# Kernel tuning notes

Hardware: AMD Instinct MI355X
Metric: run time of the kernel (lower is better)

## Reference

```python
import jax, jax.numpy as jnp
import numpy as np

D_MODEL = 1024
NUM_HEADS = 16
HEAD_DIM = D_MODEL // NUM_HEADS
LN_EPS = 1e-3  # keras LayerNormalization default epsilon


def setup_inputs() -> dict:
    key = jax.random.key(0)
    ks = jax.random.split(key, 10)
    B, T = 2, 2048
    s = 1.0 / np.sqrt(D_MODEL)
    return {
        "x": jax.random.normal(ks[0], (B, T, D_MODEL), dtype=jnp.float32),
        "Wq": jax.random.normal(ks[1], (D_MODEL, D_MODEL), dtype=jnp.float32) * s,
        "Wk": jax.random.normal(ks[2], (D_MODEL, D_MODEL), dtype=jnp.float32) * s,
        "Wv": jax.random.normal(ks[3], (D_MODEL, D_MODEL), dtype=jnp.float32) * s,
        "Wg": jax.random.normal(ks[4], (D_MODEL, D_MODEL), dtype=jnp.float32) * s,
        "bg": jnp.zeros((D_MODEL,), dtype=jnp.float32),
        "Wo": jax.random.normal(ks[5], (D_MODEL, D_MODEL), dtype=jnp.float32) * s,
        "bo": jnp.zeros((D_MODEL,), dtype=jnp.float32),
        "ln_gamma": jnp.ones((D_MODEL,), dtype=jnp.float32),
        "ln_beta": jnp.zeros((D_MODEL,), dtype=jnp.float32),
    }


def reference(x, Wq, Wk, Wv, Wg, bg, Wo, bo, ln_gamma, ln_beta):
    B, T, D = x.shape
    H, dh = NUM_HEADS, HEAD_DIM

    def split_heads(z):
        return z.reshape(B, T, H, dh).transpose(0, 2, 1, 3)  # [B,H,T,dh]

    Q = split_heads(x @ Wq)
    K = split_heads(x @ Wk)
    V = split_heads(x @ Wv)
    G = jax.nn.swish(x @ Wg + bg)  # [B,T,D]

    # Per-head causal decay mask D[h,m,n] = gamma_h^(m-n) for m>=n else 0
    idx = jnp.arange(T, dtype=jnp.float32)
    diff = idx[:, None] - idx[None, :]  # [T,T]
    causal = (diff >= 0).astype(jnp.float32)
    gammas = 1.0 - 2.0 ** (-5.0 - jnp.arange(H, dtype=jnp.float32))  # [H]
    Dmask = (gammas[:, None, None] ** jnp.maximum(diff, 0.0)) * causal  # [H,T,T]

    scale = float(dh) ** 0.5
    scores = jnp.einsum('bhtd,bhsd->bhts', Q, K) / scale  # [B,H,T,T]
    ret = jnp.einsum('bhts,bhsd->bhtd', scores * Dmask[None], V)  # [B,H,T,dh]
    ret = ret.transpose(0, 2, 1, 3).reshape(B, T, D)  # concat heads

    # LayerNorm (axis=-1, keras default eps=1e-3)
    mu = jnp.mean(ret, axis=-1, keepdims=True)
    var = jnp.mean(jnp.square(ret - mu), axis=-1, keepdims=True)
    ln = (ret - mu) / jnp.sqrt(var + LN_EPS) * ln_gamma + ln_beta

    return (ln * G) @ Wo + bo
```

## Files before the change

### kernel.cpp

```cpp
#include <hip/hip_runtime.h>

#define D_MODEL 1024
#define NHEADS  16
#define HDIM    64
#define BATCH   2
#define SEQ     2048
#define ROWS    (BATCH*SEQ)
#define CHUNK   128
#define NCHUNK  (SEQ/CHUNK)
#define LN_EPS  1e-3f

typedef unsigned short ushort_t;
typedef __attribute__((ext_vector_type(4))) float          f32x4;
typedef __attribute__((ext_vector_type(8))) short          s16x8;
typedef __attribute__((ext_vector_type(4))) unsigned short u16x4;
typedef __attribute__((ext_vector_type(8))) unsigned short u16x8;

__device__ __forceinline__ ushort_t f2b(float f) {
    union { float f; unsigned int u; } v; v.f = f;
    unsigned int r = v.u + 0x7fffu + ((v.u >> 16) & 1u);
    return (ushort_t)(r >> 16);
}
__device__ __forceinline__ float b2f(ushort_t b) {
    union { unsigned int u; float f; } v; v.u = ((unsigned int)b) << 16;
    return v.f;
}

__device__ __forceinline__ void async_load16(const ushort_t* g, ushort_t* l) {
    __builtin_amdgcn_global_load_lds(
        (const __attribute__((address_space(1))) unsigned int*)(g),
        (__attribute__((address_space(3))) unsigned int*)(l),
        16, 0, 0);
}

__global__ __launch_bounds__(256) void cast_x_kernel(const float* __restrict__ x,
                                                     ushort_t* __restrict__ xb) {
    int idx = (blockIdx.x * 256 + threadIdx.x) * 4;
    f32x4 v = *(const f32x4*)(x + idx);
    u16x4 o;
    o.x = f2b(v.x); o.y = f2b(v.y); o.z = f2b(v.z); o.w = f2b(v.w);
    *(u16x4*)(xb + idx) = o;
}

__global__ __launch_bounds__(256) void wt_transpose_kernel(
        const float* __restrict__ Wq, const float* __restrict__ Wk,
        const float* __restrict__ Wv, const float* __restrict__ Wg,
        const float* __restrict__ Wo,
        ushort_t* __restrict__ WcatT, ushort_t* __restrict__ WoT) {
    __shared__ float tile[32][33];
    int z = blockIdx.z;
    const float* W = (z == 0) ? Wq : (z == 1) ? Wk : (z == 2) ? Wv : (z == 3) ? Wg : Wo;
    ushort_t* dst = (z < 4) ? (WcatT + (size_t)z * 1024 * 1024) : WoT;
    int n0 = blockIdx.x * 32, k0 = blockIdx.y * 32;
    int tx = threadIdx.x, ty = threadIdx.y;
#pragma unroll
    for (int i = 0; i < 4; i++) {
        int k = k0 + ty + i * 8;
        tile[ty + i * 8][tx] = W[(size_t)k * 1024 + n0 + tx];
    }
    __syncthreads();
#pragma unroll
    for (int i = 0; i < 4; i++) {
        int n = n0 + ty + i * 8;
        dst[(size_t)n * 1024 + k0 + tx] = f2b(tile[tx][ty + i * 8]);
    }
}

__global__ __launch_bounds__(256, 2) void gemm_kernel(
        const ushort_t* __restrict__ A, const ushort_t* __restrict__ BT,
        int K, int N, int mode, const float* __restrict__ bias,
        ushort_t* __restrict__ Yout, float* __restrict__ Fout) {
    extern __shared__ char smem[];
    ushort_t* As = (ushort_t*)smem;
    ushort_t* Bs = As + 128 * 64;
    int t = threadIdx.x;
    int row0 = blockIdx.y * 128, col0 = blockIdx.x * 128;
    int w = t >> 6, lane = t & 63;
    int wr = (w >> 1) * 64, wc = (w & 1) * 64;
    int qd = lane >> 4, ln = lane & 15;
    int lx = ln & 7;

    f32x4 acc[4][4];
#pragma unroll
    for (int i = 0; i < 4; i++)
#pragma unroll
        for (int j = 0; j < 4; j++) acc[i][j] = (f32x4)0.0f;

    for (int k0 = 0; k0 < K; k0 += 64) {
#pragma unroll
        for (int p = 0; p < 4; p++) {
            int g = p * 256 + t;
            int r = g >> 3;
            int kb = g & 7;
            int kbs = kb ^ (r & 7);
            async_load16(A + (size_t)(row0 + r) * K + k0 + kbs * 8, As + g * 8);
            async_load16(BT + (size_t)(col0 + r) * K + k0 + kbs * 8, Bs + g * 8);
        }
        __syncthreads();
#pragma unroll
        for (int kk = 0; kk < 64; kk += 32) {
            s16x8 af[4], bf[4];
            int kxa = ((kk >> 3) + qd) ^ lx;
#pragma unroll
            for (int i = 0; i < 4; i++)
                af[i] = *(const s16x8*)(As + (wr + i * 16 + ln) * 64 + kxa * 8);
#pragma unroll
            for (int j = 0; j < 4; j++)
                bf[j] = *(const s16x8*)(Bs + (wc + j * 16 + ln) * 64 + kxa * 8);
#pragma unroll
            for (int i = 0; i < 4; i++)
#pragma unroll
                for (int j = 0; j < 4; j++)
                    acc[i][j] = __builtin_amdgcn_mfma_f32_16x16x32_bf16(
                        af[i], bf[j], acc[i][j], 0, 0, 0);
        }
        __syncthreads();
    }

#pragma unroll
    for (int i = 0; i < 4; i++)
#pragma unroll
        for (int j = 0; j < 4; j++) {
            int n = col0 + wc + j * 16 + ln;
#pragma unroll
            for (int r = 0; r < 4; r++) {
                int m = row0 + wr + i * 16 + qd * 4 + r;
                float v = acc[i][j][r];
                if (mode == 0) {
                    int region = n >> 10;
                    if (region == 0) v *= 0.125f;
                    else if (region == 3) {
                        v += bias[n & 1023];
                        v = v / (1.0f + __expf(-v));
                    }
                    Yout[(size_t)m * N + n] = f2b(v);
                } else {
                    Fout[(size_t)m * N + n] = v + bias[n];
                }
            }
        }
}

#define SJ 136
__global__ __launch_bounds__(256) void chunk_states_kernel(const ushort_t* __restrict__ Y,
                                                           float* __restrict__ Astate) {
    __shared__ ushort_t Ktd[64 * SJ];
    __shared__ ushort_t Vtd[64 * SJ];
    int c = blockIdx.x, h = blockIdx.y, b = blockIdx.z;
    int t = threadIdx.x;
    float gamma = 1.0f - exp2f(-5.0f - (float)h);
    float l2g = log2f(gamma);
    int row0 = b * SEQ + c * CHUNK;
    int colK = D_MODEL + h * HDIM;

    for (int g = t; g < 1024; g += 256) {
        int j = g >> 3, dg = (g & 7) * 8;
        size_t src = (size_t)(row0 + j) * 4096 + colK + dg;
        u16x8 k8 = *(const u16x8*)(Y + src);
        u16x8 v8 = *(const u16x8*)(Y + src + D_MODEL);
        float dec = exp2f((float)(127 - j) * l2g);
#pragma unroll
        for (int q = 0; q < 8; q++) {
            Ktd[(dg + q) * SJ + j] = f2b(b2f(k8[q]) * dec);
            Vtd[(dg + q) * SJ + j] = v8[q];
        }
    }
    __syncthreads();

    int w = t >> 6, lane = t & 63;
    int wr = w * 16;
    int qd = lane >> 4, ln = lane & 15;

    s16x8 af[4];
#pragma unroll
    for (int ks = 0; ks < 4; ks++)
        af[ks] = *(const s16x8*)(Ktd + (wr + ln) * SJ + ks * 32 + qd * 8);

    f32x4 acc[4];
#pragma unroll
    for (int nt = 0; nt < 4; nt++) {
        acc[nt] = (f32x4)0.0f;
#pragma unroll
        for (int ks = 0; ks < 4; ks++) {
            s16x8 bf = *(const s16x8*)(Vtd + (nt * 16 + ln) * SJ + ks * 32 + qd * 8);
            acc[nt] = __builtin_amdgcn_mfma_f32_16x16x32_bf16(af[ks], bf, acc[nt], 0, 0, 0);
        }
    }

    size_t base = ((size_t)((b * NHEADS + h) * NCHUNK + c)) * 4096;
#pragma unroll
    for (int nt = 0; nt < 4; nt++)
#pragma unroll
        for (int r = 0; r < 4; r++)
            Astate[base + (size_t)(wr + qd * 4 + r) * 64 + nt * 16 + ln] = acc[nt][r];
}

__global__ __launch_bounds__(256) void scan_kernel(const float* __restrict__ Astate,
                                                   float* __restrict__ Sprev) {
    int h = blockIdx.x, b = blockIdx.y;
    int bh = b * NHEADS + h;
    float gamma = 1.0f - exp2f(-5.0f - (float)h);
    float gC = exp2f(128.0f * log2f(gamma));
    for (int g = threadIdx.x; g < 1024; g += 256) {
        f32x4 S = (f32x4)0.0f;
        for (int c = 0; c < NCHUNK; c++) {
            size_t off = ((size_t)bh * NCHUNK + c) * 4096 + g * 4;
            *(f32x4*)(Sprev + off) = S;
            f32x4 Ain = *(const f32x4*)(Astate + off);
            S = S * gC + Ain;
        }
    }
}

#define LDW 72
#define VT_LDW 136
#define CO_ELEMS (128*LDW*2 + 64*LDW*2 + 64*VT_LDW)
__global__ __launch_bounds__(256, 2) void chunk_out_kernel(const ushort_t* __restrict__ Y,
                                                           const float* __restrict__ Sprev,
                                                           float* __restrict__ ret) {
    extern __shared__ char smem[];
    ushort_t* Qs   = (ushort_t*)smem;
    ushort_t* Kc   = Qs + 128 * LDW;
    ushort_t* Sphi = Kc + 128 * LDW;
    ushort_t* Splo = Sphi + 64 * LDW;
    ushort_t* Vt   = Splo + 64 * LDW;
    ushort_t* Pl   = Qs;

    int c = blockIdx.x, h = blockIdx.y, b = blockIdx.z;
    int t = threadIdx.x;
    float gamma = 1.0f - exp2f(-5.0f - (float)h);
    float l2g = log2f(gamma);
    int row0 = b * SEQ + c * CHUNK;

    for (int g = t; g < 1024; g += 256) {
        int i = g >> 3, dg = (g & 7) * 8;
        size_t src = (size_t)(row0 + i) * 4096 + h * HDIM + dg;
        *(u16x8*)(Qs + i * LDW + dg) = *(const u16x8*)(Y + src);
        *(u16x8*)(Kc + i * LDW + dg) = *(const u16x8*)(Y + src + D_MODEL);
        u16x8 v = *(const u16x8*)(Y + src + 2 * D_MODEL);
#pragma unroll
        for (int k2 = 0; k2 < 8; k2++) Vt[(dg + k2) * VT_LDW + i] = v[k2];
    }
    {
        size_t sbase = ((size_t)((b * NHEADS + h) * NCHUNK + c)) * 4096;
        for (int g = t; g < 1024; g += 256) {
            int e = g >> 4, dg = (g & 15) * 4;
            f32x4 s4 = *(const f32x4*)(Sprev + sbase + e * 64 + dg);
#pragma unroll
            for (int k2 = 0; k2 < 4; k2++) {
                float s = s4[k2];
                ushort_t hb = f2b(s);
                float lo = s - b2f(hb);
                Sphi[(dg + k2) * LDW + e] = hb;
                Splo[(dg + k2) * LDW + e] = f2b(lo);
            }
        }
    }
    __syncthreads();

    int w = t >> 6, lane = t & 63;
    int wr = w * 32;
    int qd = lane >> 4, ln = lane & 15;

    s16x8 aq[2][2];
#pragma unroll
    for (int mt = 0; mt < 2; mt++)
#pragma unroll
        for (int ks = 0; ks < 2; ks++)
            aq[mt][ks] = *(const s16x8*)(Qs + (wr + mt * 16 + ln) * LDW + ks * 32 + qd * 8);

    float prow[2][4], pcolm[8];
#pragma unroll
    for (int mt = 0; mt < 2; mt++)
#pragma unroll
        for (int r = 0; r < 4; r++)
            prow[mt][r] = exp2f((float)(wr + mt * 16 + qd * 4 + r + 1) * l2g);
#pragma unroll
    for (int nt = 0; nt < 8; nt++)
        pcolm[nt] = exp2f(-(float)(nt * 16 + ln + 1) * l2g);

    f32x4 out[2][4];
#pragma unroll
    for (int mt = 0; mt < 2; mt++)
#pragma unroll
        for (int dt = 0; dt < 4; dt++) out[mt][dt] = (f32x4)0.0f;
#pragma unroll
    for (int dt = 0; dt < 4; dt++)
#pragma unroll
        for (int ks = 0; ks < 2; ks++) {
            s16x8 bh_ = *(const s16x8*)(Sphi + (dt * 16 + ln) * LDW + ks * 32 + qd * 8);
            s16x8 bl_ = *(const s16x8*)(Splo + (dt * 16 + ln) * LDW + ks * 32 + qd * 8);
#pragma unroll
            for (int mt = 0; mt < 2; mt++) {
                out[mt][dt] = __builtin_amdgcn_mfma_f32_16x16x32_bf16(
                    aq[mt][ks], bh_, out[mt][dt], 0, 0, 0);
                out[mt][dt] = __builtin_amdgcn_mfma_f32_16x16x32_bf16(
                    aq[mt][ks], bl_, out[mt][dt], 0, 0, 0);
            }
        }
#pragma unroll
    for (int mt = 0; mt < 2; mt++)
#pragma unroll
        for (int dt = 0; dt < 4; dt++)
#pragma unroll
            for (int r = 0; r < 4; r++) out[mt][dt][r] *= prow[mt][r];

    f32x4 sc[2][8];
#pragma unroll
    for (int mt = 0; mt < 2; mt++)
#pragma unroll
        for (int nt = 0; nt < 8; nt++) sc[mt][nt] = (f32x4)0.0f;
#pragma unroll
    for (int nt = 0; nt < 8; nt++)
#pragma unroll
        for (int ks = 0; ks < 2; ks++) {
            s16x8 bk = *(const s16x8*)(Kc + (nt * 16 + ln) * LDW + ks * 32 + qd * 8);
#pragma unroll
            for (int mt = 0; mt < 2; mt++)
                sc[mt][nt] = __builtin_amdgcn_mfma_f32_16x16x32_bf16(
                    aq[mt][ks], bk, sc[mt][nt], 0, 0, 0);
        }
    __syncthreads();

#pragma unroll
    for (int mt = 0; mt < 2; mt++)
#pragma unroll
        for (int nt = 0; nt < 8; nt++) {
            int j = nt * 16 + ln;
#pragma unroll
            for (int r = 0; r < 4; r++) {
                int i = wr + mt * 16 + qd * 4 + r;
                float v = (j <= i) ? sc[mt][nt][r] * (prow[mt][r] * pcolm[nt]) : 0.0f;
                Pl[i * VT_LDW + j] = f2b(v);
            }
        }
    __syncthreads();

#pragma unroll
    for (int ks = 0; ks < 4; ks++) {
        s16x8 ap[2];
#pragma unroll
        for (int mt = 0; mt < 2; mt++)
            ap[mt] = *(const s16x8*)(Pl + (wr + mt * 16 + ln) * VT_LDW + ks * 32 + qd * 8);
#pragma unroll
        for (int dt = 0; dt < 4; dt++) {
            s16x8 bv = *(const s16x8*)(Vt + (dt * 16 + ln) * VT_LDW + ks * 32 + qd * 8);
#pragma unroll
            for (int mt = 0; mt < 2; mt++)
                out[mt][dt] = __builtin_amdgcn_mfma_f32_16x16x32_bf16(
                    ap[mt], bv, out[mt][dt], 0, 0, 0);
        }
    }

#pragma unroll
    for (int mt = 0; mt < 2; mt++)
#pragma unroll
        for (int dt = 0; dt < 4; dt++)
#pragma unroll
            for (int r = 0; r < 4; r++) {
                int i = wr + mt * 16 + qd * 4 + r;
                ret[(size_t)(row0 + i) * D_MODEL + h * HDIM + dt * 16 + ln] = out[mt][dt][r];
            }
}

__global__ __launch_bounds__(256) void ln_gate_kernel(const float* __restrict__ ret,
                                                      const ushort_t* __restrict__ Y,
                                                      const float* __restrict__ lgam,
                                                      const float* __restrict__ lbet,
                                                      ushort_t* __restrict__ LNG) {
    int row = blockIdx.x, t = threadIdx.x;
    f32x4 v = *(const f32x4*)(ret + (size_t)row * D_MODEL + t * 4);
    float s  = v.x + v.y + v.z + v.w;
    float sq = v.x * v.x + v.y * v.y + v.z * v.z + v.w * v.w;
#pragma unroll
    for (int m = 1; m < 64; m <<= 1) {
        s  += __shfl_xor(s, m);
        sq += __shfl_xor(sq, m);
    }
    __shared__ float red[8];
    int w = t >> 6, lane = t & 63;
    if (lane == 0) { red[w * 2] = s; red[w * 2 + 1] = sq; }
    __syncthreads();
    s  = red[0] + red[2] + red[4] + red[6];
    sq = red[1] + red[3] + red[5] + red[7];
    float mu  = s * (1.0f / 1024.0f);
    float var = sq * (1.0f / 1024.0f) - mu * mu;
    float inv = rsqrtf(var + LN_EPS);
    int col = t * 4;
    u16x4 ug = *(const u16x4*)(Y + (size_t)row * 4096 + 3 * D_MODEL + col);
    u16x4 o;
    o.x = f2b(((v.x - mu) * inv * lgam[col + 0] + lbet[col + 0]) * b2f(ug.x));
    o.y = f2b(((v.y - mu) * inv * lgam[col + 1] + lbet[col + 1]) * b2f(ug.y));
    o.z = f2b(((v.z - mu) * inv * lgam[col + 2] + lbet[col + 2]) * b2f(ug.z));
    o.w = f2b(((v.w - mu) * inv * lgam[col + 3] + lbet[col + 3]) * b2f(ug.w));
    *(u16x4*)(LNG + (size_t)row * D_MODEL + col) = o;
}

extern "C" void kernel_launch(void* const* d_in, const int* in_sizes, int n_in,
                              void* d_out, int out_size, void* d_ws, size_t ws_size,
                              hipStream_t stream) {
    const float* x   = (const float*)d_in[0];
    const float* Wq  = (const float*)d_in[1];
    const float* Wk  = (const float*)d_in[2];
    const float* Wv  = (const float*)d_in[3];
    const float* Wg  = (const float*)d_in[4];
    const float* bg  = (const float*)d_in[5];
    const float* Wo  = (const float*)d_in[6];
    const float* bo  = (const float*)d_in[7];
    const float* lng = (const float*)d_in[8];
    const float* lnb = (const float*)d_in[9];
    float* out = (float*)d_out;

    char* ws = (char*)d_ws;
    ushort_t* xb    = (ushort_t*)(ws);
    ushort_t* WcatT = (ushort_t*)(ws + (8ull  << 20));
    ushort_t* WoT   = (ushort_t*)(ws + (16ull << 20));
    ushort_t* Yb    = (ushort_t*)(ws + (18ull << 20));
    float*    retb  = (float*)   (ws + (50ull << 20));
    float*    Ast   = (float*)   (ws + (66ull << 20));
    float*    Sprv  = (float*)   (ws + (74ull << 20));
    ushort_t* LNGb  = (ushort_t*)(ws + (82ull << 20));

    const int GEMM_LDS = 2 * 128 * 64 * 2;
    const int CO_BYTES = CO_ELEMS * 2;

    hipFuncSetAttribute(reinterpret_cast<const void*>(gemm_kernel),
                        hipFuncAttributeMaxDynamicSharedMemorySize, GEMM_LDS);
    hipFuncSetAttribute(reinterpret_cast<const void*>(chunk_out_kernel),
                        hipFuncAttributeMaxDynamicSharedMemorySize, CO_BYTES);

    cast_x_kernel<<<ROWS * D_MODEL / 1024, 256, 0, stream>>>(x, xb);
    wt_transpose_kernel<<<dim3(32, 32, 5), dim3(32, 8), 0, stream>>>(
        Wq, Wk, Wv, Wg, Wo, WcatT, WoT);

    gemm_kernel<<<dim3(32, 32), 256, GEMM_LDS, stream>>>(
        xb, WcatT, 1024, 4096, 0, bg, Yb, (float*)nullptr);

    chunk_states_kernel<<<dim3(NCHUNK, NHEADS, BATCH), 256, 0, stream>>>(Yb, Ast);
    scan_kernel<<<dim3(NHEADS, BATCH), 256, 0, stream>>>(Ast, Sprv);
    chunk_out_kernel<<<dim3(NCHUNK, NHEADS, BATCH), 256, CO_BYTES, stream>>>(
        Yb, Sprv, retb);

    ln_gate_kernel<<<ROWS, 256, 0, stream>>>(retb, Yb, lng, lnb, LNGb);

    gemm_kernel<<<dim3(8, 32), 256, GEMM_LDS, stream>>>(
        LNGb, WoT, 1024, 1024, 1, bo, (ushort_t*)nullptr, out);
}
```

Baseline: 204.9 us.

## Merge prep kernels, vectorize LDS transposes, and parallelize the chunk-state scan

Merges the x cast and weight transpose into one launch, which removes a kernel launch. The K/V transposes into LDS in chunk_states and chunk_out are rewritten as packed 4-element writes with an XOR-swizzled order. This is meant to cut scalar LDS stores and bank conflicts. chunk_states now stores the state transposed, with the MFMA operands swapped, so that chunk_out can write Sphi/Splo as contiguous vectors. The scan is spread over 8x more blocks with 128 threads each, to raise parallelism on a small, latency-bound serial loop.

After: 203.7 us. No clear change (-0.6%).

```diff
diff --git a/kernel.cpp b/kernel.cpp
--- a/kernel.cpp
+++ b/kernel.cpp
@@ -33,26 +33,31 @@
         16, 0, 0);
 }
 
-__global__ __launch_bounds__(256) void cast_x_kernel(const float* __restrict__ x,
-                                                     ushort_t* __restrict__ xb) {
-    int idx = (blockIdx.x * 256 + threadIdx.x) * 4;
-    f32x4 v = *(const f32x4*)(x + idx);
-    u16x4 o;
-    o.x = f2b(v.x); o.y = f2b(v.y); o.z = f2b(v.z); o.w = f2b(v.w);
-    *(u16x4*)(xb + idx) = o;
-}
-
-__global__ __launch_bounds__(256) void wt_transpose_kernel(
+__global__ __launch_bounds__(256) void prep_kernel(
+        const float* __restrict__ x,
         const float* __restrict__ Wq, const float* __restrict__ Wk,
         const float* __restrict__ Wv, const float* __restrict__ Wg,
         const float* __restrict__ Wo,
-        ushort_t* __restrict__ WcatT, ushort_t* __restrict__ WoT) {
+        ushort_t* __restrict__ xb, ushort_t* __restrict__ WcatT,
+        ushort_t* __restrict__ WoT) {
     __shared__ float tile[32][33];
-    int z = blockIdx.z;
+    int bid = blockIdx.x, t = threadIdx.x;
+    if (bid < 4096) {
+        int idx = (bid * 256 + t) * 4;
+        f32x4 v = *(const f32x4*)(x + idx);
+        u16x4 o;
+        o.x = f2b(v.x); o.y = f2b(v.y); o.z = f2b(v.z); o.w = f2b(v.w);
+        *(u16x4*)(xb + idx) = o;
+        return;
+    }
+    int zb = bid - 4096;
+    int z = zb >> 10;
+    int rem = zb & 1023;
+    int bx = rem & 31, by = rem >> 5;
     const float* W = (z == 0) ? Wq : (z == 1) ? Wk : (z == 2) ? Wv : (z == 3) ? Wg : Wo;
     ushort_t* dst = (z < 4) ? (WcatT + (size_t)z * 1024 * 1024) : WoT;
-    int n0 = blockIdx.x * 32, k0 = blockIdx.y * 32;
-    int tx = threadIdx.x, ty = threadIdx.y;
+    int n0 = bx * 32, k0 = by * 32;
+    int tx = t & 31, ty = t >> 5;
 #pragma unroll
     for (int i = 0; i < 4; i++) {
         int k = k0 + ty + i * 8;
@@ -153,16 +158,29 @@
     int row0 = b * SEQ + c * CHUNK;
     int colK = D_MODEL + h * HDIM;
 
-    for (int g = t; g < 1024; g += 256) {
-        int j = g >> 3, dg = (g & 7) * 8;
-        size_t src = (size_t)(row0 + j) * 4096 + colK + dg;
-        u16x8 k8 = *(const u16x8*)(Y + src);
-        u16x8 v8 = *(const u16x8*)(Y + src + D_MODEL);
-        float dec = exp2f((float)(127 - j) * l2g);
+    {
+        int dgi = t & 7, jg = t >> 3;
+        u16x8 k8[4], v8[4];
+        float dec[4];
+#pragma unroll
+        for (int r = 0; r < 4; r++) {
+            int j = jg * 4 + r;
+            size_t src = (size_t)(row0 + j) * 4096 + colK + dgi * 8;
+            k8[r] = *(const u16x8*)(Y + src);
+            v8[r] = *(const u16x8*)(Y + src + D_MODEL);
+            dec[r] = exp2f((float)(127 - j) * l2g);
+        }
 #pragma unroll
         for (int q = 0; q < 8; q++) {
-            Ktd[(dg + q) * SJ + j] = f2b(b2f(k8[q]) * dec);
-            Vtd[(dg + q) * SJ + j] = v8[q];
+            int qq = q ^ dgi;
+            u16x4 pk, pv;
+#pragma unroll
+            for (int r = 0; r < 4; r++) {
+                pk[r] = f2b(b2f(k8[r][qq]) * dec[r]);
+                pv[r] = v8[r][qq];
+            }
+            *(u16x4*)(Ktd + (dgi * 8 + qq) * SJ + jg * 4) = pk;
+            *(u16x4*)(Vtd + (dgi * 8 + qq) * SJ + jg * 4) = pv;
         }
     }
     __syncthreads();
@@ -174,7 +192,7 @@
     s16x8 af[4];
 #pragma unroll
     for (int ks = 0; ks < 4; ks++)
-        af[ks] = *(const s16x8*)(Ktd + (wr + ln) * SJ + ks * 32 + qd * 8);
+        af[ks] = *(const s16x8*)(Vtd + (wr + ln) * SJ + ks * 32 + qd * 8);
 
     f32x4 acc[4];
 #pragma unroll
@@ -182,7 +200,7 @@
         acc[nt] = (f32x4)0.0f;
 #pragma unroll
         for (int ks = 0; ks < 4; ks++) {
-            s16x8 bf = *(const s16x8*)(Vtd + (nt * 16 + ln) * SJ + ks * 32 + qd * 8);
+            s16x8 bf = *(const s16x8*)(Ktd + (nt * 16 + ln) * SJ + ks * 32 + qd * 8);
             acc[nt] = __builtin_amdgcn_mfma_f32_16x16x32_bf16(af[ks], bf, acc[nt], 0, 0, 0);
         }
     }
@@ -195,20 +213,19 @@
             Astate[base + (size_t)(wr + qd * 4 + r) * 64 + nt * 16 + ln] = acc[nt][r];
 }
 
-__global__ __launch_bounds__(256) void scan_kernel(const float* __restrict__ Astate,
+__global__ __launch_bounds__(128) void scan_kernel(const float* __restrict__ Astate,
                                                    float* __restrict__ Sprev) {
     int h = blockIdx.x, b = blockIdx.y;
     int bh = b * NHEADS + h;
     float gamma = 1.0f - exp2f(-5.0f - (float)h);
     float gC = exp2f(128.0f * log2f(gamma));
-    for (int g = threadIdx.x; g < 1024; g += 256) {
-        f32x4 S = (f32x4)0.0f;
-        for (int c = 0; c < NCHUNK; c++) {
-            size_t off = ((size_t)bh * NCHUNK + c) * 4096 + g * 4;
-            *(f32x4*)(Sprev + off) = S;
-            f32x4 Ain = *(const f32x4*)(Astate + off);
-            S = S * gC + Ain;
-        }
+    int g = blockIdx.z * 128 + threadIdx.x;
+    size_t base = (size_t)bh * NCHUNK * 4096 + g * 4;
+    f32x4 S = (f32x4)0.0f;
+    for (int c = 0; c < NCHUNK; c++) {
+        *(f32x4*)(Sprev + base + (size_t)c * 4096) = S;
+        f32x4 Ain = *(const f32x4*)(Astate + base + (size_t)c * 4096);
+        S = S * gC + Ain;
     }
 }
 
@@ -237,23 +254,37 @@
         size_t src = (size_t)(row0 + i) * 4096 + h * HDIM + dg;
         *(u16x8*)(Qs + i * LDW + dg) = *(const u16x8*)(Y + src);
         *(u16x8*)(Kc + i * LDW + dg) = *(const u16x8*)(Y + src + D_MODEL);
-        u16x8 v = *(const u16x8*)(Y + src + 2 * D_MODEL);
-#pragma unroll
-        for (int k2 = 0; k2 < 8; k2++) Vt[(dg + k2) * VT_LDW + i] = v[k2];
+    }
+    {
+        int dgi = t & 7, jg = t >> 3;
+        u16x8 v8[4];
+#pragma unroll
+        for (int r = 0; r < 4; r++)
+            v8[r] = *(const u16x8*)(Y + (size_t)(row0 + jg * 4 + r) * 4096
+                                      + 2 * D_MODEL + h * HDIM + dgi * 8);
+#pragma unroll
+        for (int q = 0; q < 8; q++) {
+            int qq = q ^ dgi;
+            u16x4 pv;
+#pragma unroll
+            for (int r = 0; r < 4; r++) pv[r] = v8[r][qq];
+            *(u16x4*)(Vt + (dgi * 8 + qq) * VT_LDW + jg * 4) = pv;
+        }
     }
     {
         size_t sbase = ((size_t)((b * NHEADS + h) * NCHUNK + c)) * 4096;
         for (int g = t; g < 1024; g += 256) {
-            int e = g >> 4, dg = (g & 15) * 4;
-            f32x4 s4 = *(const f32x4*)(Sprev + sbase + e * 64 + dg);
+            int d = g >> 4, e0 = (g & 15) * 4;
+            f32x4 s4 = *(const f32x4*)(Sprev + sbase + d * 64 + e0);
+            u16x4 hi4, lo4;
 #pragma unroll
             for (int k2 = 0; k2 < 4; k2++) {
-                float s = s4[k2];
-                ushort_t hb = f2b(s);
-                float lo = s - b2f(hb);
-                Sphi[(dg + k2) * LDW + e] = hb;
-                Splo[(dg + k2) * LDW + e] = f2b(lo);
-            }
+                ushort_t hb = f2b(s4[k2]);
+                hi4[k2] = hb;
+                lo4[k2] = f2b(s4[k2] - b2f(hb));
+            }
+            *(u16x4*)(Sphi + d * LDW + e0) = hi4;
+            *(u16x4*)(Splo + d * LDW + e0) = lo4;
         }
     }
     __syncthreads();
@@ -429,15 +460,13 @@
     hipFuncSetAttribute(reinterpret_cast<const void*>(chunk_out_kernel),
                         hipFuncAttributeMaxDynamicSharedMemorySize, CO_BYTES);
 
-    cast_x_kernel<<<ROWS * D_MODEL / 1024, 256, 0, stream>>>(x, xb);
-    wt_transpose_kernel<<<dim3(32, 32, 5), dim3(32, 8), 0, stream>>>(
-        Wq, Wk, Wv, Wg, Wo, WcatT, WoT);
+    prep_kernel<<<4096 + 5120, 256, 0, stream>>>(x, Wq, Wk, Wv, Wg, Wo, xb, WcatT, WoT);
 
     gemm_kernel<<<dim3(32, 32), 256, GEMM_LDS, stream>>>(
         xb, WcatT, 1024, 4096, 0, bg, Yb, (float*)nullptr);
 
     chunk_states_kernel<<<dim3(NCHUNK, NHEADS, BATCH), 256, 0, stream>>>(Yb, Ast);
-    scan_kernel<<<dim3(NHEADS, BATCH), 256, 0, stream>>>(Ast, Sprv);
+    scan_kernel<<<dim3(NHEADS, BATCH, 8), 128, 0, stream>>>(Ast, Sprv);
     chunk_out_kernel<<<dim3(NCHUNK, NHEADS, BATCH), 256, CO_BYTES, stream>>>(
         Yb, Sprv, retb);
 
```
